# Kernel optimization log

Hardware: AMD Instinct MI355X
Metric: run time of the kernel (lower is better)

The kernel has to match this reference:

```python
import jax, jax.numpy as jnp
import numpy as np

TOTAL_WORDS = 10000
EMBED_LEN = 100
SEQ_LEN = 80
BATCH = 2048
UNITS = 1024


def setup_inputs() -> dict:
    key = jax.random.key(0)
    ks = jax.random.split(key, 8)
    inputs = jax.random.randint(ks[0], (BATCH, SEQ_LEN), 0, TOTAL_WORDS)
    s = 0.02
    emb = jax.random.normal(ks[1], (TOTAL_WORDS, EMBED_LEN), jnp.float32) * s
    W0 = jax.random.normal(ks[2], (EMBED_LEN, 4 * UNITS), jnp.float32) * s
    U0 = jax.random.normal(ks[3], (UNITS, 4 * UNITS), jnp.float32) * s
    b0 = jnp.zeros((4 * UNITS,), jnp.float32)
    W1 = jax.random.normal(ks[4], (UNITS, 4 * UNITS), jnp.float32) * s
    U1 = jax.random.normal(ks[5], (UNITS, 4 * UNITS), jnp.float32) * s
    b1 = jnp.zeros((4 * UNITS,), jnp.float32)
    fcW = jax.random.normal(ks[6], (UNITS, 1), jnp.float32) * s
    fcb = jnp.zeros((1,), jnp.float32)
    return {"inputs": inputs, "emb": emb, "W0": W0, "U0": U0, "b0": b0,
            "W1": W1, "U1": U1, "b1": b1, "fcW": fcW, "fcb": fcb}


def _lstm_step(x, h, c, W, U, b):
    # Keras LSTMCell gate order: i, f, g(candidate), o
    z = x @ W + h @ U + b  # [B, 4*units]
    i, f, g, o = jnp.split(z, 4, axis=-1)
    i = jax.nn.sigmoid(i)
    f = jax.nn.sigmoid(f)
    g = jnp.tanh(g)
    o = jax.nn.sigmoid(o)
    c_new = f * c + i * g
    h_new = o * jnp.tanh(c_new)
    return h_new, c_new


def reference(inputs, emb, W0, U0, b0, W1, U1, b1, fcW, fcb):
    x = emb[inputs]                      # [B, T, E]
    xs = jnp.transpose(x, (1, 0, 2))     # [T, B, E] for scan over time
    B = inputs.shape[0]
    U = U0.shape[0]
    init = (jnp.zeros((B, U), x.dtype), jnp.zeros((B, U), x.dtype),
            jnp.zeros((B, U), x.dtype), jnp.zeros((B, U), x.dtype))

    def step(carry, xt):
        h0, c0, h1, c1 = carry
        h0, c0 = _lstm_step(xt, h0, c0, W0, U0, b0)
        h1, c1 = _lstm_step(h0, h1, c1, W1, U1, b1)
        return (h0, c0, h1, c1), None

    (h0, c0, h1, c1), _ = jax.lax.scan(step, init, xs)
    logits = h1 @ fcW + fcb              # [B, 1]
    return jax.nn.sigmoid(logits)
```

## Files before the change

### kernel.cpp

```cpp
#include <hip/hip_runtime.h>

#define DEVI __device__ __forceinline__

typedef __attribute__((ext_vector_type(4))) float f4;
typedef long long i64t;
typedef __attribute__((ext_vector_type(2))) long long i64x2;

DEVI unsigned char f2fp8(float x) {
  int p = __builtin_amdgcn_cvt_pk_fp8_f32(x, x, 0, false);
  return (unsigned char)(p & 0xff);
}
DEVI float fp82f(unsigned char b) {
  return __builtin_amdgcn_cvt_f32_fp8((int)b, 0);
}
DEVI float sigmoidf_(float x) { return 1.f / (1.f + __expf(-x)); }
DEVI float tanhf_(float x) {
  float ax = fabsf(x);
  float e = __expf(-2.f * ax);
  float t = (1.f - e) / (1.f + e);
  return x < 0.f ? -t : t;
}

#define GLDS16(g, l) __builtin_amdgcn_global_load_lds( \
    (const __attribute__((address_space(1))) void*)(g), \
    (__attribute__((address_space(3))) void*)(l), 16, 0, 0)

#define SCALE_UP 64.0f
#define SCALE_DN (1.0f / 4096.0f)

DEVI int mapcol(int k, int r) {
  int c2 = ((k >> 3) & 3) ^ ((r >> 1) & 3);
  return (k & ~63) | (c2 << 4) | (((k >> 5) & 1) << 3) | (k & 7);
}


__global__ void k_conv_emb(const float* __restrict__ emb, unsigned char* __restrict__ ep) {
  int i = blockIdx.x * 256 + threadIdx.x;
  if (i >= 10000 * 128) return;
  int r = i >> 7, c = i & 127;
  ep[r * 128 + mapcol(c, 0)] =
      (c < 100) ? f2fp8(emb[r * 100 + c] * SCALE_UP) : (unsigned char)0;
}

DEVI int permn(int n) {
  int g = n >> 10, u = n & 1023;
  return (u >> 5) * 128 + ((u >> 4) & 1) * 64 + g * 16 + (u & 15);
}

__global__ void k_conv_w0(const float* __restrict__ W0, const float* __restrict__ U0,
                          unsigned char* __restrict__ WT) {
  int i = blockIdx.x * 256 + threadIdx.x;
  if (i >= 4096 * 1152) return;
  int n = i / 1152, k = i - n * 1152;
  float v;
  if (k < 100) v = W0[k * 4096 + n];
  else if (k < 128) v = 0.f;
  else v = U0[(k - 128) * 4096 + n];
  int np = permn(n);
  WT[(size_t)np * 1152 + mapcol(k, np)] = f2fp8(v * SCALE_UP);
}

__global__ void k_conv_w1(const float* __restrict__ W1, const float* __restrict__ U1,
                          unsigned char* __restrict__ WT) {
  int i = blockIdx.x * 256 + threadIdx.x;
  if (i >= 4096 * 2048) return;
  int n = i >> 11, k = i & 2047;
  float v = (k < 1024) ? W1[k * 4096 + n] : U1[(k - 1024) * 4096 + n];
  int np = permn(n);
  WT[(size_t)np * 2048 + mapcol(k, np)] = f2fp8(v * SCALE_UP);
}


template<int K1, int KTOT, bool GATHER>
DEVI void lstm_body(int blk, char* smem,
    const unsigned char* __restrict__ src1,
    const unsigned char* __restrict__ src2,
    const int* __restrict__ idx, int t,
    const unsigned char* __restrict__ WT,
    const float* __restrict__ bias,
    float* __restrict__ cbuf,
    unsigned char* __restrict__ hout)
{
  const int tid = threadIdx.x;
  const int bn = blk & 31;
  const int bm = blk >> 5;
  const int m0 = bm * 128;
  const int n0 = bn * 128;

  const int lr = tid >> 2;
  const int c16 = (tid & 3) * 16;
  const int csw = ((tid & 3) ^ ((tid >> 3) & 3)) * 16;

  const unsigned char* g1[2];
  if (GATHER) {
#pragma unroll
    for (int p = 0; p < 2; ++p) {
      int w = idx[(m0 + p * 64 + lr) * 80 + t];
      g1[p] = src1 + (size_t)w * K1 + csw;
    }
  }

  char* const LA0 = smem;
  char* const LB0 = smem + 8192;
  char* const LA1 = smem + 16384;
  char* const LB1 = smem + 24576;

  auto stage = [&](int kb) {
    char* la = (kb & 1) ? LA1 : LA0;
    char* lb = (kb & 1) ? LB1 : LB0;
    const int kc = kb * 64;
    if (GATHER && kc < K1) {
#pragma unroll
      for (int p = 0; p < 2; ++p)
        GLDS16(g1[p] + kc, la + p * 4096 + tid * 16);
    } else {
#pragma unroll
      for (int p = 0; p < 2; ++p) {
        size_t row = (size_t)(m0 + p * 64 + lr);
        const unsigned char* g = (kc < K1)
            ? (src1 + row * 1024 + kc + c16)
            : (src2 + row * 1024 + (kc - K1) + c16);
        GLDS16(g, la + p * 4096 + tid * 16);
      }
    }
#pragma unroll
    for (int p = 0; p < 2; ++p)
      GLDS16(WT + (size_t)(n0 + p * 64 + lr) * KTOT + kc + c16,
             lb + p * 4096 + tid * 16);
  };

  const int lane = tid & 63;
  const int wv = tid >> 6;
  const int wm = wv >> 1;
  const int wn = wv & 1;
  const int cl = lane & 15;
  const int qd = lane >> 4;
  const int fcl = (cl >> 1) & 3;
  const int aoff = (wm * 64 + cl) * 64 + ((qd ^ fcl) << 4);
  const int boff = (wn * 64 + cl) * 64 + ((qd ^ fcl) << 4);

  f4 acc[4][4];
  const f4 fz = {0.f, 0.f, 0.f, 0.f};
#pragma unroll
  for (int a = 0; a < 4; ++a)
#pragma unroll
    for (int b = 0; b < 4; ++b) acc[a][b] = fz;

  stage(0);

  constexpr int NKB = KTOT / 64;
#pragma unroll 1
  for (int kb = 0; kb < NKB; ++kb) {
    __syncthreads();
    if (kb + 1 < NKB) stage(kb + 1);
    char* la = (kb & 1) ? LA1 : LA0;
    char* lb = (kb & 1) ? LB1 : LB0;
    i64x2 av[4], bv[4];
#pragma unroll
    for (int mi = 0; mi < 4; ++mi)
      av[mi] = *(const i64x2*)(la + aoff + mi * 1024);
#pragma unroll
    for (int j = 0; j < 4; ++j)
      bv[j] = *(const i64x2*)(lb + boff + j * 1024);
#pragma unroll
    for (int mi = 0; mi < 4; ++mi)
#pragma unroll
      for (int j = 0; j < 4; ++j)
        acc[mi][j] = __builtin_amdgcn_mfma_f32_16x16x32_fp8_fp8(
            av[mi][0], bv[j][0], acc[mi][j], 0, 0, 0);
#pragma unroll
    for (int mi = 0; mi < 4; ++mi)
#pragma unroll
      for (int j = 0; j < 4; ++j)
        acc[mi][j] = __builtin_amdgcn_mfma_f32_16x16x32_fp8_fp8(
            av[mi][1], bv[j][1], acc[mi][j], 0, 0, 0);
  }

  const int u = bn * 32 + wn * 16 + cl;
  const int hbase = (u & ~63) | (((u >> 5) & 1) << 3) | (u & 7);
  const int c1u = (u >> 3) & 3;
  const float bi = bias[u];
  const float bff = bias[1024 + u];
  const float bg = bias[2048 + u];
  const float bo = bias[3072 + u];
#pragma unroll
  for (int mi = 0; mi < 4; ++mi) {
    int mbase = m0 + wm * 64 + mi * 16 + qd * 4;
#pragma unroll
    for (int r = 0; r < 4; ++r) {
      int m = mbase + r;
      float gi = sigmoidf_(acc[mi][0][r] * SCALE_DN + bi);
      float gf = sigmoidf_(acc[mi][1][r] * SCALE_DN + bff);
      float gg = tanhf_(acc[mi][2][r] * SCALE_DN + bg);
      float go = sigmoidf_(acc[mi][3][r] * SCALE_DN + bo);
      size_t coff = (size_t)m * 1024 + u;
      float cn = gf * cbuf[coff] + gi * gg;
      cbuf[coff] = cn;
      int c2 = c1u ^ ((qd * 2 + (r >> 1)) & 3);
      hout[(size_t)m * 1024 + (hbase | (c2 << 4))] =
          f2fp8(go * tanhf_(cn) * SCALE_UP);
    }
  }
}

__global__ __launch_bounds__(256, 4) void k_step(
    int mode,
    const unsigned char* embp, const unsigned char* h0in,
    const int* idx, int t,
    const unsigned char* WT0, const float* b0, float* c0, unsigned char* h0out,
    const unsigned char* h0prev, const unsigned char* h1in,
    const unsigned char* WT1, const float* b1, float* c1, unsigned char* h1out)
{
  extern __shared__ char smem[];
  const int blk = blockIdx.x;
  const int tile = (mode == 1) ? (blk >> 1) : blk;
  const bool isL0 = (mode == 0) || (mode == 1 && (blk & 1));
  if (isL0)
    lstm_body<128, 1152, true>(tile, smem, embp, h0in, idx, t,
                               WT0, b0, c0, h0out);
  else
    lstm_body<1024, 2048, false>(tile, smem, h0prev, h1in, nullptr, 0,
                                 WT1, b1, c1, h1out);
}


__global__ void k_fc(const unsigned char* __restrict__ h1,
                     const float* __restrict__ fcW, const float* __restrict__ fcb,
                     float* __restrict__ out) {
  int wv = threadIdx.x >> 6;
  int lane = threadIdx.x & 63;
  int row = blockIdx.x * 4 + wv;
  if (row >= 2048) return;
  const unsigned char* hr = h1 + (size_t)row * 1024;
  float s = 0.f;
  for (int k = lane; k < 1024; k += 64)
    s += fp82f(hr[mapcol(k, row)]) * fcW[k];
#pragma unroll
  for (int off = 32; off > 0; off >>= 1) s += __shfl_down(s, off);
  if (lane == 0) out[row] = sigmoidf_(s * (1.0f / SCALE_UP) + fcb[0]);
}


extern "C" void kernel_launch(void* const* d_in, const int* in_sizes, int n_in,
                              void* d_out, int out_size, void* d_ws, size_t ws_size,
                              hipStream_t stream) {
  const int*   idx = (const int*)d_in[0];
  const float* emb = (const float*)d_in[1];
  const float* W0  = (const float*)d_in[2];
  const float* U0  = (const float*)d_in[3];
  const float* b0  = (const float*)d_in[4];
  const float* W1  = (const float*)d_in[5];
  const float* U1  = (const float*)d_in[6];
  const float* b1  = (const float*)d_in[7];
  const float* fcW = (const float*)d_in[8];
  const float* fcb = (const float*)d_in[9];
  float* out = (float*)d_out;

  char* ws = (char*)d_ws;
  unsigned char* embp = (unsigned char*)(ws);
  unsigned char* WT0  = (unsigned char*)(ws + 1280000);
  unsigned char* WT1  = (unsigned char*)(ws + 5998592);
  unsigned char* h0b[2] = {(unsigned char*)(ws + 14387200),
                           (unsigned char*)(ws + 16484352)};
  unsigned char* h1b[2] = {(unsigned char*)(ws + 18581504),
                           (unsigned char*)(ws + 20678656)};
  float* c0 = (float*)(ws + 22775808);
  float* c1 = (float*)(ws + 31164416);

  hipMemsetAsync(ws + 14387200, 0, 25165824, stream);

  k_conv_emb<<<5000, 256, 0, stream>>>(emb, embp);
  k_conv_w0<<<18432, 256, 0, stream>>>(W0, U0, WT0);
  k_conv_w1<<<32768, 256, 0, stream>>>(W1, U1, WT1);

  k_step<<<512, 256, 32768, stream>>>(0, embp, h0b[1], idx, 0,
                                      WT0, b0, c0, h0b[0],
                                      nullptr, nullptr, WT1, b1, c1, nullptr);
  for (int t = 1; t < 80; ++t) {
    k_step<<<1024, 256, 32768, stream>>>(1, embp, h0b[(t + 1) & 1], idx, t,
                                         WT0, b0, c0, h0b[t & 1],
                                         h0b[(t - 1) & 1], h1b[t & 1],
                                         WT1, b1, c1, h1b[(t + 1) & 1]);
  }
  k_step<<<512, 256, 32768, stream>>>(2, nullptr, nullptr, nullptr, 0,
                                      WT0, b0, c0, nullptr,
                                      h0b[1], h1b[0], WT1, b1, c1, h1b[1]);

  k_fc<<<512, 256, 0, stream>>>(h1b[1], fcW, fcb, out);
}
```

Baseline: 4.316 ms.

## Triple-buffer LDS staging with prefetch depth two and explicit vmcnt waits

Replaces the double-buffered global-to-LDS pipeline in the LSTM GEMM body with a three-slot ring that prefetches two k-blocks ahead. __syncthreads is replaced by explicit s_waitcnt vmcnt plus s_barrier, so loads for the next block can stay in flight while the current one is consumed. The next stage is issued after the LDS fragments are read, which is meant to hide more global latency behind the MFMAs. In exchange, LDS per block grows to 48KB and launch bounds drop to 3 blocks per CU, which lowers occupancy.

New measurement: 6.290 ms. 1.46x slower.

```diff
diff --git a/kernel.cpp b/kernel.cpp
--- a/kernel.cpp
+++ b/kernel.cpp
@@ -3,7 +3,6 @@
 #define DEVI __device__ __forceinline__
 
 typedef __attribute__((ext_vector_type(4))) float f4;
-typedef long long i64t;
 typedef __attribute__((ext_vector_type(2))) long long i64x2;
 
 DEVI unsigned char f2fp8(float x) {
@@ -100,14 +99,12 @@
     }
   }
 
-  char* const LA0 = smem;
-  char* const LB0 = smem + 8192;
-  char* const LA1 = smem + 16384;
-  char* const LB1 = smem + 24576;
-
-  auto stage = [&](int kb) {
-    char* la = (kb & 1) ? LA1 : LA0;
-    char* lb = (kb & 1) ? LB1 : LB0;
+  char* const sA[3] = {smem, smem + 8192, smem + 16384};
+  char* const sB[3] = {smem + 24576, smem + 32768, smem + 40960};
+
+  auto stage = [&](int kb, int buf) {
+    char* la = sA[buf];
+    char* lb = sB[buf];
     const int kc = kb * 64;
     if (GATHER && kc < K1) {
 #pragma unroll
@@ -146,15 +143,21 @@
 #pragma unroll
     for (int b = 0; b < 4; ++b) acc[a][b] = fz;
 
-  stage(0);
-
   constexpr int NKB = KTOT / 64;
+
+  stage(0, 0);
+  stage(1, 1);
+
+  int cur = 0;
 #pragma unroll 1
   for (int kb = 0; kb < NKB; ++kb) {
-    __syncthreads();
-    if (kb + 1 < NKB) stage(kb + 1);
-    char* la = (kb & 1) ? LA1 : LA0;
-    char* lb = (kb & 1) ? LB1 : LB0;
+    if (kb + 1 < NKB)
+      asm volatile("s_waitcnt vmcnt(4)" ::: "memory");
+    else
+      asm volatile("s_waitcnt vmcnt(0)" ::: "memory");
+    asm volatile("s_barrier" ::: "memory");
+    char* la = sA[cur];
+    char* lb = sB[cur];
     i64x2 av[4], bv[4];
 #pragma unroll
     for (int mi = 0; mi < 4; ++mi)
@@ -162,6 +165,11 @@
 #pragma unroll
     for (int j = 0; j < 4; ++j)
       bv[j] = *(const i64x2*)(lb + boff + j * 1024);
+    if (kb + 2 < NKB) {
+      int nb = cur + 2;
+      if (nb >= 3) nb -= 3;
+      stage(kb + 2, nb);
+    }
 #pragma unroll
     for (int mi = 0; mi < 4; ++mi)
 #pragma unroll
@@ -174,6 +182,7 @@
       for (int j = 0; j < 4; ++j)
         acc[mi][j] = __builtin_amdgcn_mfma_f32_16x16x32_fp8_fp8(
             av[mi][1], bv[j][1], acc[mi][j], 0, 0, 0);
+    cur = (cur + 1 == 3) ? 0 : cur + 1;
   }
 
   const int u = bn * 32 + wn * 16 + cl;
@@ -203,7 +212,7 @@
   }
 }
 
-__global__ __launch_bounds__(256, 4) void k_step(
+__global__ __launch_bounds__(256, 3) void k_step(
     int mode,
     const unsigned char* embp, const unsigned char* h0in,
     const int* idx, int t,
@@ -273,16 +282,16 @@
   k_conv_w0<<<18432, 256, 0, stream>>>(W0, U0, WT0);
   k_conv_w1<<<32768, 256, 0, stream>>>(W1, U1, WT1);
 
-  k_step<<<512, 256, 32768, stream>>>(0, embp, h0b[1], idx, 0,
+  k_step<<<512, 256, 49152, stream>>>(0, embp, h0b[1], idx, 0,
                                       WT0, b0, c0, h0b[0],
                                       nullptr, nullptr, WT1, b1, c1, nullptr);
   for (int t = 1; t < 80; ++t) {
-    k_step<<<1024, 256, 32768, stream>>>(1, embp, h0b[(t + 1) & 1], idx, t,
+    k_step<<<1024, 256, 49152, stream>>>(1, embp, h0b[(t + 1) & 1], idx, t,
                                          WT0, b0, c0, h0b[t & 1],
                                          h0b[(t - 1) & 1], h1b[t & 1],
                                          WT1, b1, c1, h1b[(t + 1) & 1]);
   }
-  k_step<<<512, 256, 32768, stream>>>(2, nullptr, nullptr, nullptr, 0,
+  k_step<<<512, 256, 49152, stream>>>(2, nullptr, nullptr, nullptr, 0,
                                       WT0, b0, c0, nullptr,
                                       h0b[1], h1b[0], WT1, b1, c1, h1b[1]);
 
```
